# Kernel optimization log

Hardware: AMD Instinct MI355X
Metric: run time of the kernel (lower is better)

Reference implementation:

```python
import jax, jax.numpy as jnp
import numpy as np
from jax import lax

R = 3.0            # search_range (std of random-search perturbation)
THRESH = 1.05      # UPDATE_MULTIPLIER_THRESHOLD


def _score(coords, corr):
    """Bilinear sample each leading-dim element's own corr map at its coord.
    coords: (..., 2) with [..., 0]=x (width), [..., 1]=y (height)
    corr:   (..., H, W) with matching leading dims. Zero padding outside.
    Returns (...,) scores. Matches RAFT bilinear_sampler + grid_sample(align_corners=True)."""
    H, W = corr.shape[-2], corr.shape[-1]
    lead = coords.shape[:-1]
    c = coords.reshape(-1, 2)
    v = corr.reshape(-1, H, W)
    n = jnp.arange(v.shape[0])
    x, y = c[:, 0], c[:, 1]
    x0 = jnp.floor(x)
    y0 = jnp.floor(y)
    wx1 = x - x0
    wy1 = y - y0

    def tap(xi, yi, w):
        valid = (xi >= 0) & (xi <= W - 1) & (yi >= 0) & (yi <= H - 1)
        xc = jnp.clip(xi, 0, W - 1).astype(jnp.int32)
        yc = jnp.clip(yi, 0, H - 1).astype(jnp.int32)
        return w * jnp.where(valid, v[n, yc, xc], 0.0)

    s = (tap(x0, y0, (1 - wx1) * (1 - wy1))
         + tap(x0 + 1, y0, wx1 * (1 - wy1))
         + tap(x0, y0 + 1, (1 - wx1) * wy1)
         + tap(x0 + 1, y0 + 1, wx1 * wy1))
    return s.reshape(lead)


def _clamp(c, H, W):
    return jnp.stack([jnp.clip(c[..., 0], 0.0, W - 1.0),
                      jnp.clip(c[..., 1], 0.0, H - 1.0)], axis=-1)


def _propagate(coords, corr, dy, dx):
    """PatchMatch propagation sweep in direction (dy, dx) (equivalent of the
    custom matching_prop CUDA kernel). Sequential raster sweep: each pixel
    adopts top-neighbor coords + (0,dy) or left-neighbor coords + (dx,0) if
    the bilinear-sampled correlation score improves.
    coords: (B,H,W,2), corr: (B,H,W,H,W)."""
    B, H, W = coords.shape[:3]
    c, cm = coords, corr
    if dy < 0:
        c = jnp.flip(c, 1)
        cm = jnp.flip(cm, 1)
    if dx < 0:
        c = jnp.flip(c, 2)
        cm = jnp.flip(cm, 2)
    rows = jnp.moveaxis(c, 1, 0)        # (H,B,W,2)
    corr_rows = jnp.moveaxis(cm, 1, 0)  # (H,B,W,H,W)
    voff = jnp.array([0.0, float(dy)], dtype=c.dtype)
    hoff = jnp.array([float(dx), 0.0], dtype=c.dtype)

    def col_step(prev, xs):
        cpx, corr_px, spx, j = xs       # (B,2), (B,H,W), (B,), ()
        hc = _clamp(prev + hoff, H, W)
        hs = _score(hc, corr_px)
        u = (hs > spx) & (j > 0)
        new = jnp.where(u[:, None], hc, cpx)
        return new, new

    def row_step(prev_row, xs):
        cur, corr_row, i = xs           # (B,W,2), (B,W,H,W), ()
        cs = _score(cur, corr_row)      # (B,W)
        vc = _clamp(prev_row + voff, H, W)
        vs = _score(vc, corr_row)
        u = (vs > cs) & (i > 0)
        cur = jnp.where(u[..., None], vc, cur)
        cs = jnp.where(u, vs, cs)
        xs_cols = (jnp.moveaxis(cur, 1, 0), jnp.moveaxis(corr_row, 1, 0),
                   cs.T, jnp.arange(W))
        _, out = lax.scan(col_step, jnp.zeros((B, 2), cur.dtype), xs_cols)
        out = jnp.moveaxis(out, 0, 1)   # (B,W,2)
        return out, out

    _, res = lax.scan(row_step, jnp.zeros((B, W, 2), c.dtype),
                      (rows, corr_rows, jnp.arange(H)))
    res = jnp.moveaxis(res, 0, 1)       # (B,H,W,2)
    if dx < 0:
        res = jnp.flip(res, 2)
    if dy < 0:
        res = jnp.flip(res, 1)
    return res


def _random_search(coords, corr, eps):
    """Faithful port of __random_search (including sequential boundary
    assignments that overwrite BOTH coordinate channels, as in the source)."""
    H, W = coords.shape[1], coords.shape[2]
    new = coords + R * eps                 # torch.normal(coords, r)
    new = jnp.maximum(new, 0.0)            # new_coords[new_coords < 0] = 0
    new = jnp.where((new[..., 0] >= H)[..., None], float(H - 1), new)
    new = jnp.where((new[..., 1] >= W)[..., None], float(W - 1), new)
    old_s = _score(coords, corr)
    new_s = _score(new, corr)
    upd = new_s > THRESH * old_s
    return jnp.where(upd[..., None], new, coords)


def reference(raw_coords, corr_map, noise):
    # raw_coords: (B,2,H,W), corr_map: (B,H,W,H,W), noise: (3,B,H,W,2)
    coords = jnp.transpose(raw_coords, (0, 2, 3, 1))  # (B,H,W,2)
    dirs = ((1, 1), (-1, -1), (-1, 1), (1, -1))
    for k, (dy, dx) in enumerate(dirs):
        coords = _propagate(coords, corr_map, dy, dx)
        if k < 3:
            coords = _random_search(coords, corr_map, noise[k])
    return jnp.transpose(coords, (0, 3, 1, 2))        # (B,2,H,W)


def setup_inputs() -> dict:
    key = jax.random.key(0)
    k1, k2, k3 = jax.random.split(key, 3)
    B, H, W = 2, 64, 64
    raw_coords = jax.random.uniform(k1, (B, 2, H, W), dtype=jnp.float32) * (W - 1.0)
    corr_map = jax.random.uniform(k2, (B, H, W, H, W), dtype=jnp.float32)
    noise = jax.random.normal(k3, (3, B, H, W, 2), dtype=jnp.float32)
    return {"raw_coords": raw_coords, "corr_map": corr_map, "noise": noise}
```

## Files before the change

kernel.cpp:

```cpp
#include <hip/hip_runtime.h>


struct __attribute__((packed, aligned(4))) f2u { float x, y; };

__device__ __forceinline__ float clamp63(float v) {
    return fminf(fmaxf(v, 0.0f), 63.0f);
}

__device__ __forceinline__ float bsample(const float* __restrict__ m, float x, float y) {
    float x0f = floorf(x), y0f = floorf(y);
    float wx1 = __fsub_rn(x, x0f);
    float wy1 = __fsub_rn(y, y0f);
    float wx0 = __fsub_rn(1.0f, wx1);
    float wy0 = __fsub_rn(1.0f, wy1);
    int x0 = (int)x0f, y0 = (int)y0f;
    int x1 = x0 + 1, y1 = y0 + 1;
    int y1c = min(y1, 63);
    int bx = min(x0, 62);
    f2u p0 = *(const f2u*)(m + y0 * 64 + bx);
    f2u p1 = *(const f2u*)(m + y1c * 64 + bx);
    bool hi = (x0 > 62);
    float v00 = hi ? p0.y : p0.x;
    float v10 = (x1 <= 63) ? p0.y : 0.0f;
    float v01 = hi ? p1.y : p1.x;
    v01 = (y1 <= 63) ? v01 : 0.0f;
    float v11 = ((x1 <= 63) && (y1 <= 63)) ? p1.y : 0.0f;
    float t0 = __fmul_rn(__fmul_rn(wx0, wy0), v00);
    float t1 = __fmul_rn(__fmul_rn(wx1, wy0), v10);
    float t2 = __fmul_rn(__fmul_rn(wx0, wy1), v01);
    float t3 = __fmul_rn(__fmul_rn(wx1, wy1), v11);
    return __fadd_rn(__fadd_rn(__fadd_rn(t0, t1), t2), t3);
}

__global__ __launch_bounds__(1024, 1) void MatchingPropagator_65180423685702_kernel(
        const float* __restrict__ raw,
        const float* __restrict__ corr,
        const float* __restrict__ noise,
        float* __restrict__ out) {
    const int b = blockIdx.x;
    const float* __restrict__ corrb = corr + (size_t)b * 64 * 64 * 4096;
    const int tid = threadIdx.x;

    __shared__ float lx[4096];
    __shared__ float ly[4096];
    __shared__ float ls[4096];

    for (int p = tid; p < 4096; p += blockDim.x) {
        float x = raw[(size_t)b * 8192 + p];
        float y = raw[(size_t)b * 8192 + 4096 + p];
        lx[p] = x; ly[p] = y;
        ls[p] = bsample(corrb + (size_t)p * 4096, x, y);
    }
    __syncthreads();

    const int dys[4] = {1, -1, -1, 1};
    const int dxs[4] = {1, -1, 1, -1};

#pragma unroll
    for (int k = 0; k < 4; ++k) {
        const int dy = dys[k], dx = dxs[k];
        const float fdy = (float)dy, fdx = (float)dx;
        if (tid < 64) {
            const int r = tid;
            const int i = (dy > 0) ? r : 63 - r;
            const float* rowbase = corrb + (size_t)i * 64 * 4096;
            float cx = 0.0f, cy = 0.0f;
            for (int d = 0; d < 127; ++d) {
                float vnx = __shfl_up(cx, 1);
                float vny = __shfl_up(cy, 1);
                const int c = d - r;
                if (c >= 0 && c < 64) {
                    const int j = (dx > 0) ? c : 63 - c;
                    const int p = i * 64 + j;
                    const float* m = rowbase + (size_t)j * 4096;
                    float px = lx[p], py = ly[p], ps = ls[p];
                    float vcx = clamp63(vnx);
                    float vcy = clamp63(__fadd_rn(vny, fdy));
                    float hcx = clamp63(__fadd_rn(cx, fdx));
                    float hcy = clamp63(cy);
                    float vx0f = floorf(vcx), vy0f = floorf(vcy);
                    float hx0f = floorf(hcx), hy0f = floorf(hcy);
                    int vx0 = (int)vx0f, vy0 = (int)vy0f;
                    int hx0 = (int)hx0f, hy0 = (int)hy0f;
                    int vx1 = vx0 + 1, vy1 = vy0 + 1;
                    int hx1 = hx0 + 1, hy1 = hy0 + 1;
                    int vy1c = min(vy1, 63), hy1c = min(hy1, 63);
                    int vbx = min(vx0, 62), hbx = min(hx0, 62);
                    f2u A0 = *(const f2u*)(m + vy0 * 64 + vbx);
                    f2u A1 = *(const f2u*)(m + vy1c * 64 + vbx);
                    f2u B0 = *(const f2u*)(m + hy0 * 64 + hbx);
                    f2u B1 = *(const f2u*)(m + hy1c * 64 + hbx);
                    float vwx1 = __fsub_rn(vcx, vx0f), vwy1 = __fsub_rn(vcy, vy0f);
                    float vwx0 = __fsub_rn(1.0f, vwx1), vwy0 = __fsub_rn(1.0f, vwy1);
                    float hwx1 = __fsub_rn(hcx, hx0f), hwy1 = __fsub_rn(hcy, hy0f);
                    float hwx0 = __fsub_rn(1.0f, hwx1), hwy0 = __fsub_rn(1.0f, hwy1);
                    float vw00 = __fmul_rn(vwx0, vwy0), vw10 = __fmul_rn(vwx1, vwy0);
                    float vw01 = __fmul_rn(vwx0, vwy1), vw11 = __fmul_rn(vwx1, vwy1);
                    float hw00 = __fmul_rn(hwx0, hwy0), hw10 = __fmul_rn(hwx1, hwy0);
                    float hw01 = __fmul_rn(hwx0, hwy1), hw11 = __fmul_rn(hwx1, hwy1);
                    bool vhi = (vx0 > 62), hhi = (hx0 > 62);
                    float a00 = vhi ? A0.y : A0.x;
                    float a10 = (vx1 <= 63) ? A0.y : 0.0f;
                    float a01 = vhi ? A1.y : A1.x;
                    a01 = (vy1 <= 63) ? a01 : 0.0f;
                    float a11 = ((vx1 <= 63) && (vy1 <= 63)) ? A1.y : 0.0f;
                    float b00 = hhi ? B0.y : B0.x;
                    float b10 = (hx1 <= 63) ? B0.y : 0.0f;
                    float b01 = hhi ? B1.y : B1.x;
                    b01 = (hy1 <= 63) ? b01 : 0.0f;
                    float b11 = ((hx1 <= 63) && (hy1 <= 63)) ? B1.y : 0.0f;
                    float vs = __fadd_rn(__fadd_rn(__fadd_rn(
                                   __fmul_rn(vw00, a00), __fmul_rn(vw10, a10)),
                                   __fmul_rn(vw01, a01)), __fmul_rn(vw11, a11));
                    float hs = __fadd_rn(__fadd_rn(__fadd_rn(
                                   __fmul_rn(hw00, b00), __fmul_rn(hw10, b10)),
                                   __fmul_rn(hw01, b01)), __fmul_rn(hw11, b11));
                    bool uv = (vs > ps) && (r > 0);
                    float ux = uv ? vcx : px;
                    float uy = uv ? vcy : py;
                    float us = uv ? vs : ps;
                    bool uh = (hs > us) && (c > 0);
                    cx = uh ? hcx : ux;
                    cy = uh ? hcy : uy;
                    float fs = uh ? hs : us;
                    lx[p] = cx; ly[p] = cy; ls[p] = fs;
                }
            }
        }
        __syncthreads();

        if (k < 3) {
            const float* nz = noise + ((size_t)k * 2 + b) * 8192;
            for (int p = tid; p < 4096; p += blockDim.x) {
                float x = lx[p], y = ly[p], s = ls[p];
                float ex = nz[p * 2 + 0], ey = nz[p * 2 + 1];
                float nx = fmaxf(__fadd_rn(x, __fmul_rn(3.0f, ex)), 0.0f);
                float ny = fmaxf(__fadd_rn(y, __fmul_rn(3.0f, ey)), 0.0f);
                if (nx >= 64.0f) { nx = 63.0f; ny = 63.0f; }
                if (ny >= 64.0f) { nx = 63.0f; ny = 63.0f; }
                float ns = bsample(corrb + (size_t)p * 4096, nx, ny);
                if (ns > __fmul_rn(1.05f, s)) {
                    lx[p] = nx; ly[p] = ny; ls[p] = ns;
                }
            }
            __syncthreads();
        }
    }

    for (int p = tid; p < 4096; p += blockDim.x) {
        out[(size_t)b * 8192 + p] = lx[p];
        out[(size_t)b * 8192 + 4096 + p] = ly[p];
    }
}

extern "C" void kernel_launch(void* const* d_in, const int* in_sizes, int n_in,
                              void* d_out, int out_size, void* d_ws, size_t ws_size,
                              hipStream_t stream) {
    const float* raw   = (const float*)d_in[0];
    const float* corr  = (const float*)d_in[1];
    const float* noise = (const float*)d_in[2];
    float* out = (float*)d_out;
    (void)in_sizes; (void)n_in; (void)out_size; (void)d_ws; (void)ws_size;
    MatchingPropagator_65180423685702_kernel<<<2, 1024, 0, stream>>>(raw, corr, noise, out);
}
```

Before: 333.4 us.

## Add helper wavefronts that speculatively prefetch corr taps ahead of propagation wavefront

The block is cut from 1024 to 256 threads. Three of its four waves now act as prefetchers that follow the main propagation wave through a shared progress counter. Each prefetcher guesses the next diagonal's candidate coordinates from the current state and loads the matching correlation taps so they are in cache when the serial sweep reaches them. The goal is to hide global-memory latency on the sequential critical path. The costs are polling traffic on a volatile shared variable, extra memory bandwidth, and fewer threads for the parallel random-search and init phases.

```diff
diff --git a/kernel.cpp b/kernel.cpp
--- a/kernel.cpp
+++ b/kernel.cpp
@@ -32,7 +32,7 @@
     return __fadd_rn(__fadd_rn(__fadd_rn(t0, t1), t2), t3);
 }
 
-__global__ __launch_bounds__(1024, 1) void MatchingPropagator_65180423685702_kernel(
+__global__ __launch_bounds__(256, 1) void MatchingPropagator_65180423685702_kernel(
         const float* __restrict__ raw,
         const float* __restrict__ corr,
         const float* __restrict__ noise,
@@ -40,12 +40,15 @@
     const int b = blockIdx.x;
     const float* __restrict__ corrb = corr + (size_t)b * 64 * 64 * 4096;
     const int tid = threadIdx.x;
+    const int wid = tid >> 6;
+    const int lane = tid & 63;
 
     __shared__ float lx[4096];
     __shared__ float ly[4096];
     __shared__ float ls[4096];
-
-    for (int p = tid; p < 4096; p += blockDim.x) {
+    __shared__ volatile int prog;
+
+    for (int p = tid; p < 4096; p += 256) {
         float x = raw[(size_t)b * 8192 + p];
         float y = raw[(size_t)b * 8192 + 4096 + p];
         lx[p] = x; ly[p] = y;
@@ -60,8 +63,13 @@
     for (int k = 0; k < 4; ++k) {
         const int dy = dys[k], dx = dxs[k];
         const float fdy = (float)dy, fdx = (float)dx;
-        if (tid < 64) {
-            const int r = tid;
+        const bool dxpos = (dx > 0);
+
+        if (tid == 0) prog = -1;
+        __syncthreads();
+
+        if (wid == 0) {
+            const int r = lane;
             const int i = (dy > 0) ? r : 63 - r;
             const float* rowbase = corrb + (size_t)i * 64 * 4096;
             float cx = 0.0f, cy = 0.0f;
@@ -70,7 +78,7 @@
                 float vny = __shfl_up(cy, 1);
                 const int c = d - r;
                 if (c >= 0 && c < 64) {
-                    const int j = (dx > 0) ? c : 63 - c;
+                    const int j = dxpos ? c : 63 - c;
                     const int p = i * 64 + j;
                     const float* m = rowbase + (size_t)j * 4096;
                     float px = lx[p], py = ly[p], ps = ls[p];
@@ -125,13 +133,67 @@
                     float fs = uh ? hs : us;
                     lx[p] = cx; ly[p] = cy; ls[p] = fs;
                 }
+                if (lane == 0) prog = d;
+            }
+        } else {
+            const int sel = wid - 1;
+            const int r = lane;
+            const int i = (dy > 0) ? r : 63 - r;
+            const float* rowbase = corrb + (size_t)i * 64 * 4096;
+
+#pragma unroll 1
+            for (int t = 0; t < 126; ++t) {
+                while (prog < t - 1) __builtin_amdgcn_s_sleep(2);
+                const int cp = t + 1 - r;
+                if (cp >= 0 && cp < 64) {
+                    auto readst = [&](int rr, int cc, float& x, float& y) {
+                        rr = min(max(rr, 0), 63); cc = min(max(cc, 0), 63);
+                        int ii = (dy > 0) ? rr : 63 - rr;
+                        int jj = dxpos ? cc : 63 - cc;
+                        int pp = ii * 64 + jj;
+                        x = lx[pp]; y = ly[pp];
+                    };
+                    float kx, ky, nx, ny, ax, ay;
+                    if (sel == 0) {
+                        readst(r, cp - 1, kx, ky);
+                        readst(r - 1, cp, nx, ny);
+                    } else if (sel == 1) {
+                        readst(r - 1, cp - 1, ax, ay);
+                        kx = clamp63(ax); ky = clamp63(__fadd_rn(ay, fdy));
+                        readst(r - 2, cp, ax, ay);
+                        nx = clamp63(ax); ny = clamp63(__fadd_rn(ay, fdy));
+                    } else {
+                        readst(r, cp - 2, ax, ay);
+                        kx = clamp63(__fadd_rn(ax, fdx)); ky = clamp63(ay);
+                        readst(r - 1, cp - 1, ax, ay);
+                        nx = clamp63(__fadd_rn(ax, fdx)); ny = clamp63(ay);
+                    }
+                    float hx = clamp63(__fadd_rn(kx, fdx)), hy = clamp63(ky);
+                    float vx = clamp63(nx), vy = clamp63(__fadd_rn(ny, fdy));
+                    const int j = dxpos ? cp : 63 - cp;
+                    const float* m = rowbase + (size_t)j * 4096;
+                    {
+                        int x0 = (int)floorf(hx), y0 = (int)floorf(hy);
+                        int bx = min(x0, 62), y1c = min(y0 + 1, 63);
+                        f2u A = *(const f2u*)(m + y0 * 64 + bx);
+                        f2u B = *(const f2u*)(m + y1c * 64 + bx);
+                        asm volatile("" :: "v"(A.x), "v"(A.y), "v"(B.x), "v"(B.y));
+                    }
+                    {
+                        int x0 = (int)floorf(vx), y0 = (int)floorf(vy);
+                        int bx = min(x0, 62), y1c = min(y0 + 1, 63);
+                        f2u A = *(const f2u*)(m + y0 * 64 + bx);
+                        f2u B = *(const f2u*)(m + y1c * 64 + bx);
+                        asm volatile("" :: "v"(A.x), "v"(A.y), "v"(B.x), "v"(B.y));
+                    }
+                }
             }
         }
         __syncthreads();
 
         if (k < 3) {
             const float* nz = noise + ((size_t)k * 2 + b) * 8192;
-            for (int p = tid; p < 4096; p += blockDim.x) {
+            for (int p = tid; p < 4096; p += 256) {
                 float x = lx[p], y = ly[p], s = ls[p];
                 float ex = nz[p * 2 + 0], ey = nz[p * 2 + 1];
                 float nx = fmaxf(__fadd_rn(x, __fmul_rn(3.0f, ex)), 0.0f);
@@ -147,7 +209,7 @@
         }
     }
 
-    for (int p = tid; p < 4096; p += blockDim.x) {
+    for (int p = tid; p < 4096; p += 256) {
         out[(size_t)b * 8192 + p] = lx[p];
         out[(size_t)b * 8192 + 4096 + p] = ly[p];
     }
@@ -161,5 +223,5 @@
     const float* noise = (const float*)d_in[2];
     float* out = (float*)d_out;
     (void)in_sizes; (void)n_in; (void)out_size; (void)d_ws; (void)ws_size;
-    MatchingPropagator_65180423685702_kernel<<<2, 1024, 0, stream>>>(raw, corr, noise, out);
-}
+    MatchingPropagator_65180423685702_kernel<<<2, 256, 0, stream>>>(raw, corr, noise, out);
+}
```

Result: slower. 552.3 us (+65.6%).

## Add helper blocks that prefetch upcoming corr maps into cache ahead of the sweep

Applied to the files above, without the earlier changes.

Launches extra helper blocks that poll a progress flag in workspace memory, which the main blocks publish at every diagonal step. For the current step, each helper reads the full corr maps the main sweep will use and discards the sum, only to warm L2 or MALL. The goal is to hide the latency of the dependent 64-thread diagonal gathers, which the two active blocks leave mostly exposed. The scheme relies on spin-polling, extra memory traffic, and helpers being co-resident, and it has a bounded poll count.

```diff
diff --git a/kernel.cpp b/kernel.cpp
--- a/kernel.cpp
+++ b/kernel.cpp
@@ -32,14 +32,61 @@
     return __fadd_rn(__fadd_rn(__fadd_rn(t0, t1), t2), t3);
 }
 
+__constant__ const int c_dys[4] = {1, -1, -1, 1};
+__constant__ const int c_dxs[4] = {1, -1, 1, -1};
+
 __global__ __launch_bounds__(1024, 1) void MatchingPropagator_65180423685702_kernel(
         const float* __restrict__ raw,
         const float* __restrict__ corr,
         const float* __restrict__ noise,
-        float* __restrict__ out) {
-    const int b = blockIdx.x;
+        float* __restrict__ out,
+        int* __restrict__ ws) {
+    const int blk = blockIdx.x;
+    const int tid = threadIdx.x;
+
+    if (blk >= 2) {
+        const int wrk = blk & 7;
+        if (wrk > 1 || blk < 8) return;
+        const int rank = (blk >> 3) - 1;
+        int* flag = ws + wrk * 64;
+        const float* __restrict__ corrb = corr + (size_t)wrk * 64 * 64 * 4096;
+        int last_t = -1000;
+        int polls = 0;
+        while (polls < 300000) {
+            int v = __hip_atomic_load(flag, __ATOMIC_RELAXED, __HIP_MEMORY_SCOPE_AGENT);
+            if (v >= 512) break;
+            if (v < -2) { ++polls; __builtin_amdgcn_s_sleep(8); continue; }
+            int t = v + 2;
+            if (t == last_t) { ++polls; __builtin_amdgcn_s_sleep(2); continue; }
+            last_t = t;
+            int kt = t >> 7;
+            if (kt > 3) { ++polls; __builtin_amdgcn_s_sleep(2); continue; }
+            int dd = min(t & 127, 126);
+            const int dy = c_dys[kt], dx = c_dxs[kt];
+            const int gid = rank * 1024 + tid;
+            const int r = gid >> 6, sub = gid & 63;
+            const int c = dd - r;
+            if (c >= 0 && c < 64) {
+                const int i = (dy > 0) ? r : 63 - r;
+                const int j = (dx > 0) ? c : 63 - c;
+                const float4* mp = (const float4*)(corrb + (size_t)(i * 64 + j) * 4096);
+                float acc = 0.0f;
+#pragma unroll
+                for (int q = 0; q < 16; ++q) {
+                    float4 v4 = mp[sub + q * 64];
+                    acc += v4.x + v4.y + v4.z + v4.w;
+                }
+                asm volatile("" :: "v"(acc));
+            }
+        }
+        return;
+    }
+
+    const int b = blk;
     const float* __restrict__ corrb = corr + (size_t)b * 64 * 64 * 4096;
-    const int tid = threadIdx.x;
+    int* flag = ws + b * 64;
+    if (tid == 0)
+        __hip_atomic_store(flag, -2, __ATOMIC_RELAXED, __HIP_MEMORY_SCOPE_AGENT);
 
     __shared__ float lx[4096];
     __shared__ float ly[4096];
@@ -66,6 +113,9 @@
             const float* rowbase = corrb + (size_t)i * 64 * 4096;
             float cx = 0.0f, cy = 0.0f;
             for (int d = 0; d < 127; ++d) {
+                if (tid == 0)
+                    __hip_atomic_store(flag, k * 128 + d, __ATOMIC_RELAXED,
+                                       __HIP_MEMORY_SCOPE_AGENT);
                 float vnx = __shfl_up(cx, 1);
                 float vny = __shfl_up(cy, 1);
                 const int c = d - r;
@@ -147,6 +197,9 @@
         }
     }
 
+    if (tid == 0)
+        __hip_atomic_store(flag, 1000, __ATOMIC_RELAXED, __HIP_MEMORY_SCOPE_AGENT);
+
     for (int p = tid; p < 4096; p += blockDim.x) {
         out[(size_t)b * 8192 + p] = lx[p];
         out[(size_t)b * 8192 + 4096 + p] = ly[p];
@@ -160,6 +213,8 @@
     const float* corr  = (const float*)d_in[1];
     const float* noise = (const float*)d_in[2];
     float* out = (float*)d_out;
-    (void)in_sizes; (void)n_in; (void)out_size; (void)d_ws; (void)ws_size;
-    MatchingPropagator_65180423685702_kernel<<<2, 1024, 0, stream>>>(raw, corr, noise, out);
-}
+    int* ws = (int*)d_ws;
+    (void)in_sizes; (void)n_in; (void)out_size; (void)ws_size;
+    MatchingPropagator_65180423685702_kernel<<<34, 1024, 0, stream>>>(
+        raw, corr, noise, out, ws);
+}
```

After: 363.9 us. 1.09x slower.
